# Optimization experiments

Hardware: AMD Instinct MI355X
Metric: run time of the kernel (lower is better)

## Reference

```python
import jax, jax.numpy as jnp
import numpy as np

B, N, C = 8, 1024, 768
HEADS = 8
HD = C // HEADS  # head_dim = qk_dim // num_heads since qk_ratio=1
SCALE = HD ** (-0.5)


def setup_inputs() -> dict:
    key = jax.random.key(0)
    ks = jax.random.split(key, 8)
    s = 0.02
    return {
        "x": jax.random.normal(ks[0], (B, N, C), dtype=jnp.float32),
        "y": jax.random.normal(ks[1], (B, N, C), dtype=jnp.float32),
        "relative_pos": jax.random.normal(ks[2], (HEADS, N, N), dtype=jnp.float32),
        "H": 32,
        "W": 32,
        "Wq": jax.random.normal(ks[3], (C, C), dtype=jnp.float32) * s,
        "Wk": jax.random.normal(ks[4], (C, C), dtype=jnp.float32) * s,
        "Wv": jax.random.normal(ks[5], (C, C), dtype=jnp.float32) * s,
        "Wp": jax.random.normal(ks[6], (C, C), dtype=jnp.float32) * s,
        "bp": jnp.zeros((C,), dtype=jnp.float32),
    }


def reference(x, y, relative_pos, H, W, Wq, Wk, Wv, Wp, bp):
    # sr_ratio == 1 path: K/V come directly from y (no spatial reduction).
    b, n, c = x.shape
    q = (x @ Wq.T).reshape(b, n, HEADS, HD)       # bnhd
    k = (y @ Wk.T).reshape(b, n, HEADS, HD)       # bmhd
    v = (y @ Wv.T).reshape(b, n, HEADS, HD)       # bmhd
    # scores: QK^T * scale + learned relative position bias (broadcast over batch)
    attn = jnp.einsum("bnhd,bmhd->bhnm", q, k) * SCALE + relative_pos[None]
    attn = jax.nn.softmax(attn, axis=-1)
    out = jnp.einsum("bhnm,bmhd->bnhd", attn, v).reshape(b, n, c)
    return out @ Wp.T + bp
```

## Files before the change

### kernel.cpp

```cpp
#include <hip/hip_runtime.h>
#include <hip/hip_bf16.h>
#include <cstdint>
#include <cstddef>


using f32x4  = __attribute__((ext_vector_type(4))) float;
using bf16x8 = __attribute__((ext_vector_type(8))) __bf16;

constexpr int Bb = 8, Nn = 1024, Cc = 768;
constexpr float LOG2E = 1.4426950408889634f;
constexpr float QSC   = 0.10206207261596575f * 1.4426950408889634f;

__device__ __forceinline__ uint16_t f2bf(float f) {
  union { float f; uint32_t u; } v; v.f = f;
  return (uint16_t)((v.u + 0x7fffu + ((v.u >> 16) & 1u)) >> 16);
}

__device__ __forceinline__ void gl_lds16(const void* g, void* l) {
  __builtin_amdgcn_global_load_lds(
      (const __attribute__((address_space(1))) void*)g,
      (__attribute__((address_space(3))) void*)l, 16, 0, 0);
}

__device__ __forceinline__ f32x4 mfma16(bf16x8 a, bf16x8 b, f32x4 c) {
  return __builtin_amdgcn_mfma_f32_16x16x32_bf16(a, b, c, 0, 0, 0);
}

template <int CTRL>
__device__ __forceinline__ float dpp_max(float v) {
  union { float f; int i; } u, r;
  u.f = v;
  r.i = __builtin_amdgcn_update_dpp(u.i, u.i, CTRL, 0xF, 0xF, false);
  return fmaxf(v, r.f);
}
template <int CTRL>
__device__ __forceinline__ float dpp_add(float v) {
  union { float f; int i; } u, r;
  u.f = v;
  r.i = __builtin_amdgcn_update_dpp(u.i, u.i, CTRL, 0xF, 0xF, false);
  return v + r.f;
}
__device__ __forceinline__ float red16_max(float v) {
  v = dpp_max<0x128>(v);
  v = dpp_max<0x124>(v);
  v = dpp_max<0x122>(v);
  v = dpp_max<0x121>(v);
  return v;
}
__device__ __forceinline__ float red16_add(float v) {
  v = dpp_add<0x128>(v);
  v = dpp_add<0x124>(v);
  v = dpp_add<0x122>(v);
  v = dpp_add<0x121>(v);
  return v;
}

__global__ void cvt2_kernel(const float* __restrict__ a,
                            const float* __restrict__ b,
                            uint16_t* __restrict__ da,
                            uint16_t* __restrict__ db, int n4) {
  int i = blockIdx.x * blockDim.x + threadIdx.x;
  const float* s = blockIdx.y ? b : a;
  uint16_t* d = blockIdx.y ? db : da;
  if (i < n4) {
    float4 v = ((const float4*)s)[i];
    ushort4 o;
    o.x = f2bf(v.x); o.y = f2bf(v.y); o.z = f2bf(v.z); o.w = f2bf(v.w);
    ((ushort4*)d)[i] = o;
  }
}

__global__ void cvtw_kernel(const float* __restrict__ wq,
                            const float* __restrict__ wk,
                            const float* __restrict__ wv,
                            const float* __restrict__ wp,
                            uint16_t* __restrict__ dq, uint16_t* __restrict__ dk,
                            uint16_t* __restrict__ dv, uint16_t* __restrict__ dp,
                            int n4) {
  int i = blockIdx.x * blockDim.x + threadIdx.x;
  const float* s; uint16_t* d; float sc = 1.f;
  switch (blockIdx.y) {
    case 0:  s = wq; d = dq; sc = QSC; break;
    case 1:  s = wk; d = dk; break;
    case 2:  s = wv; d = dv; break;
    default: s = wp; d = dp; break;
  }
  if (i < n4) {
    float4 v = ((const float4*)s)[i];
    ushort4 o;
    o.x = f2bf(v.x * sc); o.y = f2bf(v.y * sc);
    o.z = f2bf(v.z * sc); o.w = f2bf(v.w * sc);
    ((ushort4*)d)[i] = o;
  }
}

__device__ __forceinline__ void gemm_core(const uint16_t* __restrict__ A,
                                          const uint16_t* __restrict__ Bt,
                                          int m0, int n0, f32x4 (&acc)[4][4]) {
  __shared__ uint16_t As[128 * 64];
  __shared__ uint16_t Bs[128 * 64];
  const int tid = threadIdx.x;
  const int lane = tid & 63, l16 = lane & 15, quad = lane >> 4;
  const int w = tid >> 6;
  const int wm = (w & 1) * 64, wn = (w >> 1) * 64;

  int soff[4];
#pragma unroll
  for (int i = 0; i < 4; ++i) {
    int idx = tid + 256 * i;
    int row = idx >> 3, pc = idx & 7;
    int c = pc ^ (row & 7);
    soff[i] = row * 768 + c * 8;
  }

  for (int k0 = 0; k0 < 768; k0 += 64) {
    __syncthreads();
#pragma unroll
    for (int i = 0; i < 4; ++i)
      gl_lds16(A + (size_t)m0 * 768 + k0 + soff[i], &As[(tid + 256 * i) * 8]);
#pragma unroll
    for (int i = 0; i < 4; ++i)
      gl_lds16(Bt + (size_t)n0 * 768 + k0 + soff[i], &Bs[(tid + 256 * i) * 8]);
    __syncthreads();

#pragma unroll
    for (int ks = 0; ks < 2; ++ks) {
      bf16x8 a[4], b[4];
      const int phys = (ks * 4 + quad) ^ (l16 & 7);
#pragma unroll
      for (int i = 0; i < 4; ++i)
        a[i] = *(const bf16x8*)&As[(wm + i * 16 + l16) * 64 + phys * 8];
#pragma unroll
      for (int j = 0; j < 4; ++j)
        b[j] = *(const bf16x8*)&Bs[(wn + j * 16 + l16) * 64 + phys * 8];
#pragma unroll
      for (int i = 0; i < 4; ++i)
#pragma unroll
        for (int j = 0; j < 4; ++j)
          acc[i][j] = mfma16(a[i], b[j], acc[i][j]);
    }
  }
}

__global__ __launch_bounds__(256, 3) void qkv_kernel(
    const uint16_t* __restrict__ xb, const uint16_t* __restrict__ yb,
    const uint16_t* __restrict__ wq, const uint16_t* __restrict__ wk,
    const uint16_t* __restrict__ wv, uint16_t* __restrict__ Qb,
    uint16_t* __restrict__ Kb, uint16_t* __restrict__ Vt) {
  const int seg = blockIdx.x / 6, nb = blockIdx.x % 6;
  const uint16_t* A  = (seg == 0) ? xb : yb;
  const uint16_t* Bt = (seg == 0) ? wq : (seg == 1) ? wk : wv;
  const int m0 = blockIdx.y * 128, n0 = nb * 128;

  f32x4 acc[4][4] = {};
  gemm_core(A, Bt, m0, n0, acc);

  const int tid = threadIdx.x, lane = tid & 63;
  const int l16 = lane & 15, quad = lane >> 4, w = tid >> 6;
  const int wm = (w & 1) * 64, wn = (w >> 1) * 64;

  if (seg <= 1) {
    uint16_t* O = seg ? Kb : Qb;
#pragma unroll
    for (int i = 0; i < 4; ++i)
#pragma unroll
      for (int j = 0; j < 4; ++j) {
        int col = n0 + wn + j * 16 + l16;
#pragma unroll
        for (int r = 0; r < 4; ++r) {
          int row = m0 + wm + i * 16 + quad * 4 + r;
          O[(size_t)row * 768 + col] = f2bf(acc[i][j][r]);
        }
      }
  } else {
#pragma unroll
    for (int i = 0; i < 4; ++i) {
      int row0 = m0 + wm + i * 16 + quad * 4;
      int bidx = row0 >> 10, nseq = row0 & 1023;
#pragma unroll
      for (int j = 0; j < 4; ++j) {
        int col = n0 + wn + j * 16 + l16;
        int h = col / 96, hd = col % 96;
        ushort4 pk;
        pk.x = f2bf(acc[i][j][0]); pk.y = f2bf(acc[i][j][1]);
        pk.z = f2bf(acc[i][j][2]); pk.w = f2bf(acc[i][j][3]);
        size_t o = (((size_t)(bidx * 8 + h) * 96 + hd) << 10) + nseq;
        *(ushort4*)(Vt + o) = pk;
      }
    }
  }
}

__global__ __launch_bounds__(256, 3) void proj_kernel(
    const uint16_t* __restrict__ A, const uint16_t* __restrict__ Bt,
    float* __restrict__ out, const float* __restrict__ bias) {
  const int m0 = blockIdx.y * 128, n0 = blockIdx.x * 128;
  f32x4 acc[4][4] = {};
  gemm_core(A, Bt, m0, n0, acc);

  const int tid = threadIdx.x, lane = tid & 63;
  const int l16 = lane & 15, quad = lane >> 4, w = tid >> 6;
  const int wm = (w & 1) * 64, wn = (w >> 1) * 64;
  float bv[4];
#pragma unroll
  for (int j = 0; j < 4; ++j) bv[j] = bias[n0 + wn + j * 16 + l16];
#pragma unroll
  for (int i = 0; i < 4; ++i)
#pragma unroll
    for (int j = 0; j < 4; ++j) {
      int col = n0 + wn + j * 16 + l16;
#pragma unroll
      for (int r = 0; r < 4; ++r) {
        int row = m0 + wm + i * 16 + quad * 4 + r;
        out[(size_t)row * 768 + col] = acc[i][j][r] + bv[j];
      }
    }
}

__global__ __launch_bounds__(256, 4) void attn_kernel(
    const uint16_t* __restrict__ Q,
    const uint16_t* __restrict__ Kb,
    const uint16_t* __restrict__ Vt,
    const float* __restrict__ rel,
    uint16_t* __restrict__ AO) {
  __shared__ uint16_t Ks[64 * 96];
  __shared__ uint16_t Vs[96 * 64];
  __shared__ uint16_t Ps[64 * 64];

  const int tid = threadIdx.x;
  const int q0 = blockIdx.x * 64;
  const int bh = blockIdx.y;
  const int b = bh >> 3, h = bh & 7;
  const int w = tid >> 6, lane = tid & 63;
  const int l16 = lane & 15, quad = lane >> 4;
  const int l7 = l16 & 7;

  const int qrow = q0 + w * 16 + l16;
  bf16x8 qf[3];
  {
    const uint16_t* qp =
        Q + ((size_t)(b * 1024 + qrow)) * 768 + h * 96 + quad * 8;
#pragma unroll
    for (int j = 0; j < 3; ++j) qf[j] = *(const bf16x8*)(qp + j * 32);
  }

  int koff[3], voff[3];
#pragma unroll
  for (int i = 0; i < 3; ++i) {
    int idx = tid + 256 * i;
    int krow = idx / 12, kpc = idx % 12;
    int kc = (kpc < 8) ? (kpc ^ (krow & 7)) : (8 + ((kpc & 3) ^ (krow & 3)));
    koff[i] = krow * 768 + kc * 8;
    int d = idx >> 3, vpc = idx & 7;
    int vc = vpc ^ (d & 7);
    voff[i] = d * 1024 + vc * 8;
  }

  float m_i[4], l_i[4];
#pragma unroll
  for (int r = 0; r < 4; ++r) { m_i[r] = -1e30f; l_i[r] = 0.f; }
  f32x4 o_acc[6] = {};

  const float* relbase =
      rel + ((size_t)h << 20) + ((size_t)(q0 + w * 16 + quad * 4) << 10) + l16;
  const uint16_t* kslab = Kb + ((size_t)(b * 1024)) * 768 + h * 96;
  const uint16_t* vslab = Vt + ((size_t)(bh * 96) << 10);

  for (int kt = 0; kt < 16; ++kt) {
    const int k0 = kt * 64;
    __syncthreads();
#pragma unroll
    for (int i = 0; i < 3; ++i)
      gl_lds16(kslab + (size_t)k0 * 768 + koff[i], &Ks[(tid + 256 * i) * 8]);
#pragma unroll
    for (int i = 0; i < 3; ++i)
      gl_lds16(vslab + k0 + voff[i], &Vs[(tid + 256 * i) * 8]);

    float relv[16];
#pragma unroll
    for (int r = 0; r < 4; ++r)
#pragma unroll
      for (int nt = 0; nt < 4; ++nt)
        relv[nt * 4 + r] = relbase[(size_t)r * 1024 + k0 + nt * 16];

    __syncthreads();

    f32x4 s[4] = {};
#pragma unroll
    for (int ksi = 0; ksi < 3; ++ksi) {
#pragma unroll
      for (int nt = 0; nt < 4; ++nt) {
        const int row = nt * 16 + l16;
        const int c = ksi * 4 + quad;
        const int phys =
            (ksi < 2) ? (c ^ (row & 7)) : (8 + ((c & 3) ^ (row & 3)));
        bf16x8 kf = *(const bf16x8*)&Ks[row * 96 + phys * 8];
        s[nt] = mfma16(qf[ksi], kf, s[nt]);
      }
    }

    float vals[16];
#pragma unroll
    for (int nt = 0; nt < 4; ++nt)
#pragma unroll
      for (int r = 0; r < 4; ++r)
        vals[nt * 4 + r] = fmaf(relv[nt * 4 + r], LOG2E, s[nt][r]);

#pragma unroll
    for (int r = 0; r < 4; ++r) {
      float mx = fmaxf(fmaxf(vals[r], vals[4 + r]),
                       fmaxf(vals[8 + r], vals[12 + r]));
      mx = red16_max(mx);
      float mnew = fmaxf(m_i[r], mx);
      float alpha = __builtin_amdgcn_exp2f(m_i[r] - mnew);
      m_i[r] = mnew;
      float p0 = __builtin_amdgcn_exp2f(vals[r] - mnew);
      float p1 = __builtin_amdgcn_exp2f(vals[4 + r] - mnew);
      float p2 = __builtin_amdgcn_exp2f(vals[8 + r] - mnew);
      float p3 = __builtin_amdgcn_exp2f(vals[12 + r] - mnew);
      vals[r] = p0; vals[4 + r] = p1; vals[8 + r] = p2; vals[12 + r] = p3;
      float rs = red16_add((p0 + p1) + (p2 + p3));
      l_i[r] = l_i[r] * alpha + rs;
#pragma unroll
      for (int jt = 0; jt < 6; ++jt) o_acc[jt][r] *= alpha;
    }

    const int khi = l16 >> 3;
#pragma unroll
    for (int r = 0; r < 4; ++r) {
      const int qloc = quad * 4 + r;
      const int rowoff = (w * 16 + qloc) * 64;
      const int sw = qloc & 7;
#pragma unroll
      for (int nt = 0; nt < 4; ++nt) {
        const int kc = 2 * nt + khi;
        Ps[rowoff + (((kc ^ sw) << 3) | l7)] = f2bf(vals[nt * 4 + r]);
      }
    }
    asm volatile("s_waitcnt lgkmcnt(0)" ::: "memory");

#pragma unroll
    for (int ksi = 0; ksi < 2; ++ksi) {
      const int c = ksi * 4 + quad;
      const int phys = c ^ l7;
      bf16x8 pf = *(const bf16x8*)&Ps[(w * 16 + l16) * 64 + phys * 8];
#pragma unroll
      for (int jt = 0; jt < 6; ++jt) {
        const int d = jt * 16 + l16;
        bf16x8 vf = *(const bf16x8*)&Vs[d * 64 + phys * 8];
        o_acc[jt] = mfma16(pf, vf, o_acc[jt]);
      }
    }
  }

#pragma unroll
  for (int r = 0; r < 4; ++r) {
    float inv = 1.f / l_i[r];
    int row = q0 + w * 16 + quad * 4 + r;
#pragma unroll
    for (int jt = 0; jt < 6; ++jt) {
      int col = h * 96 + jt * 16 + l16;
      AO[(size_t)(b * 1024 + row) * 768 + col] = f2bf(o_acc[jt][r] * inv);
    }
  }
}

extern "C" void kernel_launch(void* const* d_in, const int* in_sizes, int n_in,
                              void* d_out, int out_size, void* d_ws,
                              size_t ws_size, hipStream_t stream) {
  const float* x   = (const float*)d_in[0];
  const float* y   = (const float*)d_in[1];
  const float* rel = (const float*)d_in[2];
  const float* Wq  = (const float*)d_in[5];
  const float* Wk  = (const float*)d_in[6];
  const float* Wv  = (const float*)d_in[7];
  const float* Wp  = (const float*)d_in[8];
  const float* bp  = (const float*)d_in[9];
  float* out = (float*)d_out;

  const size_t nBNC = (size_t)Bb * Nn * Cc;
  const size_t nW = (size_t)Cc * Cc;

  char* ws = (char*)d_ws;
  size_t off = 0;
  auto alloc = [&](size_t bytes) {
    char* p = ws + off;
    off += (bytes + 255) & ~(size_t)255;
    return p;
  };
  uint16_t* xb  = (uint16_t*)alloc(nBNC * 2);
  uint16_t* yb  = (uint16_t*)alloc(nBNC * 2);
  uint16_t* wqb = (uint16_t*)alloc(nW * 2);
  uint16_t* wkb = (uint16_t*)alloc(nW * 2);
  uint16_t* wvb = (uint16_t*)alloc(nW * 2);
  uint16_t* wpb = (uint16_t*)alloc(nW * 2);
  uint16_t* Qb  = (uint16_t*)alloc(nBNC * 2);
  uint16_t* Kb  = (uint16_t*)alloc(nBNC * 2);
  uint16_t* Vtb = (uint16_t*)alloc(nBNC * 2);
  uint16_t* AOb = (uint16_t*)alloc(nBNC * 2);

  cvt2_kernel<<<dim3((int)(nBNC / 4 / 256), 2), 256, 0, stream>>>(
      x, y, xb, yb, (int)(nBNC / 4));
  cvtw_kernel<<<dim3((int)(nW / 4 / 256), 4), 256, 0, stream>>>(
      Wq, Wk, Wv, Wp, wqb, wkb, wvb, wpb, (int)(nW / 4));

  qkv_kernel<<<dim3(18, 64), 256, 0, stream>>>(xb, yb, wqb, wkb, wvb, Qb, Kb,
                                               Vtb);

  attn_kernel<<<dim3(16, 64), 256, 0, stream>>>(Qb, Kb, Vtb, rel, AOb);

  proj_kernel<<<dim3(6, 64), 256, 0, stream>>>(AOb, wpb, out, bp);
}
```

Baseline: 260.3 us.

## Double-buffer K/V tiles and bias in attention, with 128-query blocks

The attention kernel now prefetches the next K/V tile, via global-to-LDS loads, into a second LDS buffer, and loads the next relative-position bias values into registers while the current tile is computed. This removes the second barrier per iteration and overlaps memory latency with MFMA and softmax work. Blocks grow to 512 threads and 128 query rows, so each staged K/V tile is shared by more queries. The P scratch switches from an XOR swizzle to padded rows of 72. The costs are more LDS per block, which lowers how many blocks fit per CU, and higher register pressure from the doubled bias registers under the new launch bounds.

```diff
diff --git a/kernel.cpp b/kernel.cpp
--- a/kernel.cpp
+++ b/kernel.cpp
@@ -217,18 +217,18 @@
     }
 }
 
-__global__ __launch_bounds__(256, 4) void attn_kernel(
+__global__ __launch_bounds__(512, 4) void attn_kernel(
     const uint16_t* __restrict__ Q,
     const uint16_t* __restrict__ Kb,
     const uint16_t* __restrict__ Vt,
     const float* __restrict__ rel,
     uint16_t* __restrict__ AO) {
-  __shared__ uint16_t Ks[64 * 96];
-  __shared__ uint16_t Vs[96 * 64];
-  __shared__ uint16_t Ps[64 * 64];
+  __shared__ uint16_t Ks[2][64 * 96];
+  __shared__ uint16_t Vs[2][96 * 64];
+  __shared__ uint16_t Ps[128 * 72];
 
   const int tid = threadIdx.x;
-  const int q0 = blockIdx.x * 64;
+  const int q0 = blockIdx.x * 128;
   const int bh = blockIdx.y;
   const int b = bh >> 3, h = bh & 7;
   const int w = tid >> 6, lane = tid & 63;
@@ -244,46 +244,67 @@
     for (int j = 0; j < 3; ++j) qf[j] = *(const bf16x8*)(qp + j * 32);
   }
 
-  int koff[3], voff[3];
-#pragma unroll
-  for (int i = 0; i < 3; ++i) {
-    int idx = tid + 256 * i;
-    int krow = idx / 12, kpc = idx % 12;
-    int kc = (kpc < 8) ? (kpc ^ (krow & 7)) : (8 + ((kpc & 3) ^ (krow & 3)));
-    koff[i] = krow * 768 + kc * 8;
-    int d = idx >> 3, vpc = idx & 7;
-    int vc = vpc ^ (d & 7);
-    voff[i] = d * 1024 + vc * 8;
-  }
+  auto kSrc = [](int c) {
+    int r = c / 12, pc = c % 12;
+    int kc = (pc < 8) ? (pc ^ (r & 7)) : (8 + ((pc & 3) ^ (r & 3)));
+    return r * 768 + kc * 8;
+  };
+  auto vSrc = [](int c) {
+    int d = c >> 3, pc = c & 7;
+    return d * 1024 + (pc ^ (d & 7)) * 8;
+  };
+  const int  kc0 = tid;
+  const int  ks0 = kSrc(kc0);
+  const bool isK1 = (tid < 256);
+  const int  c1 = isK1 ? (512 + tid) : (tid - 256);
+  const int  s1 = isK1 ? kSrc(c1) : vSrc(c1);
+  const int  vc2 = 256 + tid;
+  const int  vs2 = vSrc(vc2);
+
+  const uint16_t* kslab = Kb + ((size_t)(b * 1024)) * 768 + h * 96;
+  const uint16_t* vslab = Vt + ((size_t)(bh * 96) << 10);
+  const float* relbase =
+      rel + ((size_t)h << 20) + ((size_t)(q0 + w * 16 + quad * 4) << 10) + l16;
+
+  auto stage = [&](int knext, int bufi) {
+    const uint16_t* kb = kslab + (size_t)knext * 768;
+    const uint16_t* vb = vslab + knext;
+    uint16_t* Kbuf = &Ks[bufi][0];
+    uint16_t* Vbuf = &Vs[bufi][0];
+    gl_lds16(kb + ks0, Kbuf + kc0 * 8);
+    if (isK1) gl_lds16(kb + s1, Kbuf + c1 * 8);
+    else      gl_lds16(vb + s1, Vbuf + c1 * 8);
+    gl_lds16(vb + vs2, Vbuf + vc2 * 8);
+  };
+
+  float relv[2][16];
+  auto loadrel = [&](int knext, float (&dst)[16]) {
+#pragma unroll
+    for (int r = 0; r < 4; ++r)
+#pragma unroll
+      for (int nt = 0; nt < 4; ++nt)
+        dst[nt * 4 + r] = relbase[(size_t)r * 1024 + knext + nt * 16];
+  };
 
   float m_i[4], l_i[4];
 #pragma unroll
   for (int r = 0; r < 4; ++r) { m_i[r] = -1e30f; l_i[r] = 0.f; }
   f32x4 o_acc[6] = {};
 
-  const float* relbase =
-      rel + ((size_t)h << 20) + ((size_t)(q0 + w * 16 + quad * 4) << 10) + l16;
-  const uint16_t* kslab = Kb + ((size_t)(b * 1024)) * 768 + h * 96;
-  const uint16_t* vslab = Vt + ((size_t)(bh * 96) << 10);
-
+  stage(0, 0);
+  loadrel(0, relv[0]);
+
+#pragma unroll 2
   for (int kt = 0; kt < 16; ++kt) {
-    const int k0 = kt * 64;
+    const int cur = kt & 1, nxt = (kt + 1) & 1;
     __syncthreads();
-#pragma unroll
-    for (int i = 0; i < 3; ++i)
-      gl_lds16(kslab + (size_t)k0 * 768 + koff[i], &Ks[(tid + 256 * i) * 8]);
-#pragma unroll
-    for (int i = 0; i < 3; ++i)
-      gl_lds16(vslab + k0 + voff[i], &Vs[(tid + 256 * i) * 8]);
-
-    float relv[16];
-#pragma unroll
-    for (int r = 0; r < 4; ++r)
-#pragma unroll
-      for (int nt = 0; nt < 4; ++nt)
-        relv[nt * 4 + r] = relbase[(size_t)r * 1024 + k0 + nt * 16];
-
-    __syncthreads();
+    if (kt < 15) {
+      stage((kt + 1) * 64, nxt);
+      loadrel((kt + 1) * 64, relv[nxt]);
+    }
+    const uint16_t* KsC = &Ks[cur][0];
+    const uint16_t* VsC = &Vs[cur][0];
+    const float* rv = relv[cur];
 
     f32x4 s[4] = {};
 #pragma unroll
@@ -294,7 +315,7 @@
         const int c = ksi * 4 + quad;
         const int phys =
             (ksi < 2) ? (c ^ (row & 7)) : (8 + ((c & 3) ^ (row & 3)));
-        bf16x8 kf = *(const bf16x8*)&Ks[row * 96 + phys * 8];
+        bf16x8 kf = *(const bf16x8*)&KsC[row * 96 + phys * 8];
         s[nt] = mfma16(qf[ksi], kf, s[nt]);
       }
     }
@@ -304,7 +325,7 @@
     for (int nt = 0; nt < 4; ++nt)
 #pragma unroll
       for (int r = 0; r < 4; ++r)
-        vals[nt * 4 + r] = fmaf(relv[nt * 4 + r], LOG2E, s[nt][r]);
+        vals[nt * 4 + r] = fmaf(rv[nt * 4 + r], LOG2E, s[nt][r]);
 
 #pragma unroll
     for (int r = 0; r < 4; ++r) {
@@ -325,29 +346,24 @@
       for (int jt = 0; jt < 6; ++jt) o_acc[jt][r] *= alpha;
     }
 
-    const int khi = l16 >> 3;
 #pragma unroll
     for (int r = 0; r < 4; ++r) {
-      const int qloc = quad * 4 + r;
-      const int rowoff = (w * 16 + qloc) * 64;
-      const int sw = qloc & 7;
-#pragma unroll
-      for (int nt = 0; nt < 4; ++nt) {
-        const int kc = 2 * nt + khi;
-        Ps[rowoff + (((kc ^ sw) << 3) | l7)] = f2bf(vals[nt * 4 + r]);
-      }
+      const int rowoff = (w * 16 + quad * 4 + r) * 72;
+#pragma unroll
+      for (int nt = 0; nt < 4; ++nt)
+        Ps[rowoff + nt * 16 + l16] = f2bf(vals[nt * 4 + r]);
     }
     asm volatile("s_waitcnt lgkmcnt(0)" ::: "memory");
 
 #pragma unroll
     for (int ksi = 0; ksi < 2; ++ksi) {
-      const int c = ksi * 4 + quad;
-      const int phys = c ^ l7;
-      bf16x8 pf = *(const bf16x8*)&Ps[(w * 16 + l16) * 64 + phys * 8];
+      bf16x8 pf =
+          *(const bf16x8*)&Ps[(w * 16 + l16) * 72 + ksi * 32 + quad * 8];
 #pragma unroll
       for (int jt = 0; jt < 6; ++jt) {
         const int d = jt * 16 + l16;
-        bf16x8 vf = *(const bf16x8*)&Vs[d * 64 + phys * 8];
+        const int phys = (ksi * 4 + quad) ^ l7;
+        bf16x8 vf = *(const bf16x8*)&VsC[d * 64 + phys * 8];
         o_acc[jt] = mfma16(pf, vf, o_acc[jt]);
       }
     }
@@ -407,7 +423,7 @@
   qkv_kernel<<<dim3(18, 64), 256, 0, stream>>>(xb, yb, wqb, wkb, wvb, Qb, Kb,
                                                Vtb);
 
-  attn_kernel<<<dim3(16, 64), 256, 0, stream>>>(Qb, Kb, Vtb, rel, AOb);
+  attn_kernel<<<dim3(8, 64), 512, 0, stream>>>(Qb, Kb, Vtb, rel, AOb);
 
   proj_kernel<<<dim3(6, 64), 256, 0, stream>>>(AOb, wpb, out, bp);
 }
```

New measurement: 272.9 us. 4.8% more time.
